# Performance work log

Measured on AMD Instinct MI355X. Metric: run time of the kernel, lower is better.

## Reference

```python
import jax, jax.numpy as jnp
import numpy as np

B, N, F_IN = 256, 256, 128
HID, DEPTH = 48, 4
D_OUT = 97                 # sum(latent_dim [32,32,32,1]) = GraphUNet out_channels
K_SORT = 30
C1, C2, KW2 = 16, 32, 5
POOL_LEN = (K_SORT - 2) // 2 + 1        # 15 after maxpool1d(2,2)
DENSE_DIM = (POOL_LEN - KW2 + 1) * C2   # 352
OUT_DIM = 32


def _gcn(x, A, W, b):
    # GCNConv(improved=True): A_hat = A + 2I; out = D^-1/2 A_hat D^-1/2 (x W) + b
    n = A.shape[-1]
    Ah = A + 2.0 * jnp.eye(n, dtype=A.dtype)
    dinv = jax.lax.rsqrt(jnp.sum(Ah, axis=-1))          # deg >= 2 always
    An = dinv[:, :, None] * Ah * dinv[:, None, :]
    return An @ (x @ W) + b


def _augment(A):
    # GraphUNet.augment_adj: add self loops, two-hop (A@A), remove self loops
    n = A.shape[-1]
    eye = jnp.eye(n, dtype=A.dtype)
    A1 = A + eye
    return (A1 @ A1) * (1.0 - eye)


def _topk_pool(x, A, p):
    # TopKPooling(ratio=0.5, nonlinearity=tanh): score = tanh(x.p/||p||)
    Bb, n, _ = x.shape
    score = jnp.tanh((x @ p) / jnp.sqrt(jnp.sum(p * p)))
    k = (n + 1) // 2
    vals, perm = jax.lax.top_k(score, k)                # [B,k]
    bidx = jnp.arange(Bb)[:, None]
    xp = x[bidx, perm] * vals[..., None]                # gate kept nodes by score
    Ap = A[bidx[..., None], perm[:, :, None], perm[:, None, :]]
    return xp, Ap, perm


def _forward(x, A, dW0, db0, dW, db, pool_p, uW, ub, uWl, ubl, c1W, c1b, c2W, c2b, oW, ob):
    act = jax.nn.relu
    # ---- GraphUNet down path ----
    h = act(_gcn(x, A, dW0, db0))
    xs, As, perms = [h], [A], []
    Acur = A
    for i in range(DEPTH):
        A2 = _augment(Acur)
        h, Acur, perm = _topk_pool(h, A2, pool_p[i])
        h = act(_gcn(h, Acur, dW[i], db[i]))
        if i < DEPTH - 1:
            xs.append(h)
            As.append(Acur)
        perms.append(perm)
    # ---- up path with sum skip connections ----
    for i in range(DEPTH):
        j = DEPTH - 1 - i
        res, Aj, perm = xs[j], As[j], perms[j]
        bidx = jnp.arange(res.shape[0])[:, None]
        up = jnp.zeros_like(res).at[bidx, perm].set(h)
        h = res + up
        if i < DEPTH - 1:
            h = act(_gcn(h, Aj, uW[i], ub[i]))
        else:
            h = _gcn(h, Aj, uWl, ubl)                   # [B,N,D_OUT], no act
    # ---- global_sort_pool: sort nodes by last channel desc, keep top K_SORT ----
    _, order = jax.lax.top_k(h[..., -1], K_SORT)
    sp = h[jnp.arange(B)[:, None], order]               # [B,K_SORT,D_OUT]
    # conv1d(1->C1, kernel=stride=D_OUT) on flattened [B,1,K*D] == per-node linear
    y = jax.nn.relu(jnp.einsum('bkd,cd->bck', sp, c1W) + c1b[None, :, None])  # [B,C1,K]
    y = y.reshape(B, C1, POOL_LEN, 2).max(-1)           # maxpool1d(2,2)
    y = jax.lax.conv_general_dilated(y, c2W, (1,), 'VALID',
                                     dimension_numbers=('NCH', 'OIH', 'NCH'))
    y = jax.nn.relu(y + c2b[None, :, None])             # [B,C2,POOL_LEN-KW2+1]
    return jax.nn.relu(y.reshape(B, -1) @ oW + ob)      # relu(relu(.)) == relu(.)


def setup_inputs():
    key = jax.random.key(0)
    ks = jax.random.split(key, 12)
    x = jax.random.normal(ks[0], (B, N, F_IN), dtype=jnp.float32)
    # symmetric binary adjacency, no self loops, avg degree ~15
    u = jax.random.uniform(ks[1], (B, N, N))
    A = (u < 0.03).astype(jnp.float32)
    A = jnp.maximum(A, A.transpose(0, 2, 1)) * (1.0 - jnp.eye(N, dtype=jnp.float32))
    s = lambda f: np.float32(1.0 / np.sqrt(f))
    return dict(
        x=x, A=A,
        dW0=jax.random.normal(ks[2], (F_IN, HID), dtype=jnp.float32) * s(F_IN),
        db0=jnp.zeros((HID,), jnp.float32),
        dW=jax.random.normal(ks[3], (DEPTH, HID, HID), dtype=jnp.float32) * s(HID),
        db=jnp.zeros((DEPTH, HID), jnp.float32),
        pool_p=jax.random.normal(ks[4], (DEPTH, HID), dtype=jnp.float32) * s(HID),
        uW=jax.random.normal(ks[5], (DEPTH - 1, HID, HID), dtype=jnp.float32) * s(HID),
        ub=jnp.zeros((DEPTH - 1, HID), jnp.float32),
        uWl=jax.random.normal(ks[6], (HID, D_OUT), dtype=jnp.float32) * s(HID),
        ubl=jnp.zeros((D_OUT,), jnp.float32),
        c1W=jax.random.normal(ks[7], (C1, D_OUT), dtype=jnp.float32) * s(D_OUT),
        c1b=jnp.zeros((C1,), jnp.float32),
        c2W=jax.random.normal(ks[8], (C2, C1, KW2), dtype=jnp.float32) * s(C1 * KW2),
        c2b=jnp.zeros((C2,), jnp.float32),
        oW=jax.random.normal(ks[9], (DENSE_DIM, OUT_DIM), dtype=jnp.float32) * s(DENSE_DIM),
        ob=jnp.zeros((OUT_DIM,), jnp.float32),
    )


def reference(x, A, dW0, db0, dW, db, pool_p, uW, ub, uWl, ubl, c1W, c1b, c2W, c2b, oW, ob):
    return _forward(x, A, dW0, db0, dW, db, pool_p, uW, ub, uWl, ubl, c1W, c1b, c2W, c2b, oW, ob)
```

## Files before the change

kernel.cpp:

```cpp
#include <hip/hip_runtime.h>
#include <math.h>

#define BATCH 256
#define NNODE 256
#define FIN   128
#define HID   48
#define DOUT  97

#define WOFF_DW0 0
#define WOFF_DW  6144
#define WOFF_UW  18432
#define WOFF_UWL 27648
#define WTOT     34816

typedef __attribute__((ext_vector_type(8))) short bf16x8_t;
typedef __attribute__((ext_vector_type(4))) float f32x4_t;

__device__ inline unsigned short f2bf(float x) {
  unsigned u = __float_as_uint(x);
  u += 0x7fff + ((u >> 16) & 1);
  return (unsigned short)(u >> 16);
}
__device__ inline float bf2f(unsigned short h) {
  return __uint_as_float(((unsigned)h) << 16);
// ... 77 lines not shown
  int mt = (blockIdx.x * 256 + threadIdx.x) >> 6;
  int lane = threadIdx.x & 63;
  int r = lane & 15, q = lane >> 4;
  const float* xr = X + ((long)mt * 16 + r) * K;
  bf16x8_t ah[KS2], am[KS2], al[KS2];
  #pragma unroll
  for (int ks = 0; ks < KS2; ks++) {
    int col0 = ks * 32 + q * 8;
    float v[8];
    if (col0 + 8 <= K) {
      float4 a = *(const float4*)(xr + col0);
      float4 b = *(const float4*)(xr + col0 + 4);
      v[0] = a.x; v[1] = a.y; v[2] = a.z; v[3] = a.w;
      v[4] = b.x; v[5] = b.y; v[6] = b.z; v[7] = b.w;
    } else {
      #pragma unroll
      for (int j = 0; j < 8; j++) v[j] = (col0 + j < K) ? xr[col0 + j] : 0.f;
    }
    #pragma unroll
    for (int j = 0; j < 8; j++) {
      unsigned short h = f2bf(v[j]);
      float r1 = v[j] - bf2f(h);
      unsigned short m = f2bf(r1);
      float r2 = r1 - bf2f(m);
      unsigned short l = f2bf(r2);
      ah[ks][j] = (short)h;
      am[ks][j] = (short)m;
      al[ks][j] = (short)l;
    }
  }
  long row0 = (long)mt * 16 + q * 4;
  float4 dv4 = {0.f, 0.f, 0.f, 0.f};
  long ytBase = 0;
  if (Yth) {
    dv4 = *(const float4*)(dinv + row0);
    int bb = (int)(row0 >> nShift);
    int jj = (int)(row0 & ((1 << nShift) - 1));
    ytBase = (long)bb * Fpad;
    ytBase = ytBase << nShift;
    ytBase += jj;
  }
  int nFT = Fpad >> 4;
  for (int ft = 0; ft < nFT; ft++) {
    int fl = ft * 16 + r;
    const unsigned short* wb = Wp + (size_t)fl * KP + q * 8;
    f32x4_t acc = {0.f, 0.f, 0.f, 0.f};
    #pragma unroll
    for (int ks = 0; ks < KS2; ks++) {
      bf16x8_t bh = *(const bf16x8_t*)(wb + ks * 32);
      bf16x8_t bm = *(const bf16x8_t*)(wb + WTOT + ks * 32);
      bf16x8_t bl = *(const bf16x8_t*)(wb + 2 * WTOT + ks * 32);
      acc = __builtin_amdgcn_mfma_f32_16x16x32_bf16(ah[ks], bh, acc, 0, 0, 0);
      acc = __builtin_amdgcn_mfma_f32_16x16x32_bf16(ah[ks], bm, acc, 0, 0, 0);
      acc = __builtin_amdgcn_mfma_f32_16x16x32_bf16(am[ks], bh, acc, 0, 0, 0);
      acc = __builtin_amdgcn_mfma_f32_16x16x32_bf16(am[ks], bm, acc, 0, 0, 0);
      acc = __builtin_amdgcn_mfma_f32_16x16x32_bf16(ah[ks], bl, acc, 0, 0, 0);
      acc = __builtin_amdgcn_mfma_f32_16x16x32_bf16(al[ks], bh, acc, 0, 0, 0);
    }
    int f = fl;
    if (f < F) {
      if (XW) {
        #pragma unroll
        for (int reg = 0; reg < 4; reg++) XW[(row0 + reg) * F + f] = acc[reg];
      }
      if (Yth) {
        float dvv[4] = {dv4.x, dv4.y, dv4.z, dv4.w};
        unsigned long long hpk = 0, lpk = 0;
        #pragma unroll
        for (int reg = 0; reg < 4; reg++) {
          float v = dvv[reg] * acc[reg];
          unsigned short hi = f2bf(v);
          unsigned short lo = f2bf(v - bf2f(hi));
          hpk |= ((unsigned long long)hi) << (16 * reg);
          lpk |= ((unsigned long long)lo) << (16 * reg);
        }
        long o = ytBase + ((long)f << nShift);
        *(unsigned long long*)(Yth + o) = hpk;
        *(unsigned long long*)(Ytl + o) = lpk;
      }
    }
  }
}

__global__ __launch_bounds__(512) void k_big(const float* __restrict__ x,
                                             const unsigned short* __restrict__ Wp0,
                                             const unsigned short* __restrict__ Abf0,
                                             const float* __restrict__ D0,
                                             const float* __restrict__ db0,
                                             float* __restrict__ H0) {
  __shared__ __align__(16) char yt0[24576];
  __shared__ __align__(16) char yt1[24576];
  int b = blockIdx.x, t = threadIdx.x;
  int w = t >> 6, lane = t & 63;
  int r = lane & 15, q = lane >> 4;
  const float* Xb = x + (size_t)b * 256 * 128;
  const float* Db = D0 + (size_t)b * 256;
  #pragma unroll
  for (int half = 0; half < 2; half++) {
    int m = w + half * 8;
    const float* xr = Xb + (size_t)(m * 16 + r) * 128;
    bf16x8_t ah[4], am[4], al[4];
    #pragma unroll
    for (int ks = 0; ks < 4; ks++) {
      int col0 = ks * 32 + q * 8;
      float4 a4 = *(const float4*)(xr + col0);
      float4 b4 = *(const float4*)(xr + col0 + 4);
      float v[8] = {a4.x, a4.y, a4.z, a4.w, b4.x, b4.y, b4.z, b4.w};
      #pragma unroll
      for (int j = 0; j < 8; j++) {
        unsigned short h = f2bf(v[j]); float r1 = v[j] - bf2f(h);
        unsigned short mm = f2bf(r1);  float r2 = r1 - bf2f(mm);
        ah[ks][j] = (short)h; am[ks][j] = (short)mm; al[ks][j] = (short)f2bf(r2);
      }
    }
    int row0 = m * 16 + q * 4;
    float4 dv4 = *(const float4*)(Db + row0);
    float dvv[4] = {dv4.x, dv4.y, dv4.z, dv4.w};
    #pragma unroll
    for (int ft = 0; ft < 3; ft++) {
      int fl = ft * 16 + r;
      const unsigned short* wb = Wp0 + (size_t)fl * 128 + q * 8;
      f32x4_t acc = {0.f, 0.f, 0.f, 0.f};
      #pragma unroll
      for (int ks = 0; ks < 4; ks++) {
        bf16x8_t bh = *(const bf16x8_t*)(wb + ks * 32);
        bf16x8_t bm = *(const bf16x8_t*)(wb + WTOT + ks * 32);
        bf16x8_t bl = *(const bf16x8_t*)(wb + 2 * WTOT + ks * 32);
        acc = __builtin_amdgcn_mfma_f32_16x16x32_bf16(ah[ks], bh, acc, 0, 0, 0);
        acc = __builtin_amdgcn_mfma_f32_16x16x32_bf16(ah[ks], bm, acc, 0, 0, 0);
        acc = __builtin_amdgcn_mfma_f32_16x16x32_bf16(am[ks], bh, acc, 0, 0, 0);
        acc = __builtin_amdgcn_mfma_f32_16x16x32_bf16(am[ks], bm, acc, 0, 0, 0);
        acc = __builtin_amdgcn_mfma_f32_16x16x32_bf16(ah[ks], bl, acc, 0, 0, 0);
        acc = __builtin_amdgcn_mfma_f32_16x16x32_bf16(al[ks], bh, acc, 0, 0, 0);
      }
      #pragma unroll
      for (int reg = 0; reg < 4; reg++) {
        float vv = dvv[reg] * acc[reg];
        unsigned short hi = f2bf(vv);
        unsigned short lo = f2bf(vv - bf2f(hi));
        int byte = (fl * 512 + (row0 + reg) * 2) ^ ((fl & 7) << 4);
        *(unsigned short*)(yt0 + byte) = hi;
        *(unsigned short*)(yt1 + byte) = lo;
      }
    }
  }
  __syncthreads();
  #pragma unroll
  for (int half = 0; half < 2; half++) {
    int it = w + half * 8;
    const unsigned short* ap = Abf0 + ((size_t)b * 256 + it * 16 + r) * 256 + q * 8;
    bf16x8_t af[8];
    #pragma unroll
    for (int ks = 0; ks < 8; ks++) af[ks] = *(const bf16x8_t*)(ap + ks * 32);
    #pragma unroll
    for (int ft = 0; ft < 3; ft++) {
      int fl = ft * 16 + r;
      f32x4_t acc = {0.f, 0.f, 0.f, 0.f};
      #pragma unroll
      for (int ks = 0; ks < 8; ks++) {
        int byte = (fl * 512 + (ks * 32 + q * 8) * 2) ^ ((fl & 7) << 4);
        bf16x8_t bh = *(const bf16x8_t*)(yt0 + byte);
        bf16x8_t bl = *(const bf16x8_t*)(yt1 + byte);
        acc = __builtin_amdgcn_mfma_f32_16x16x32_bf16(af[ks], bh, acc, 0, 0, 0);
        acc = __builtin_amdgcn_mfma_f32_16x16x32_bf16(af[ks], bl, acc, 0, 0, 0);
      }
      float bfv = db0[fl];
      #pragma unroll
      for (int reg = 0; reg < 4; reg++) {
        int rr = it * 16 + q * 4 + reg;
        int sbyte = (fl * 512 + rr * 2) ^ ((fl & 7) << 4);
        float selfv = bf2f(*(const unsigned short*)(yt0 + sbyte))
                    + bf2f(*(const unsigned short*)(yt1 + sbyte));
        float d = Db[rr];
        float v = d * acc[reg] + 2.f * d * selfv + bfv;
        H0[((size_t)b * 256 + rr) * 48 + fl] = fmaxf(v, 0.f);
      }
    }
  }
}

template<int MODE>
__device__ inline void gcn128_phase(const float* __restrict__ Xg,
                                    const unsigned short* __restrict__ Wpl,
                                    const unsigned short* __restrict__ A1,
                                    const float* __restrict__ D1b,
                                    const float* __restrict__ bias,
                                    char* yt0, char* yt1,
                                    float* __restrict__ H1,
                                    float* __restrict__ H0b,
                                    const int* sPerm1, int t) {
  int w = t >> 6, lane = t & 63;
  int r = lane & 15, q = lane >> 4;
  {
    const float* xr = Xg + (size_t)(w * 16 + r) * 48;
    bf16x8_t ah[2], am[2], al[2];
    #pragma unroll
    for (int ks = 0; ks < 2; ks++) {
      int col0 = ks * 32 + q * 8;
      float v[8];
      if (col0 + 8 <= 48) {
        float4 a4 = *(const float4*)(xr + col0);
        float4 b4 = *(const float4*)(xr + col0 + 4);
        v[0]=a4.x; v[1]=a4.y; v[2]=a4.z; v[3]=a4.w;
        v[4]=b4.x; v[5]=b4.y; v[6]=b4.z; v[7]=b4.w;
      } else {
        #pragma unroll
        for (int j = 0; j < 8; j++) v[j] = (col0 + j < 48) ? xr[col0 + j] : 0.f;
      }
      #pragma unroll
      for (int j = 0; j < 8; j++) {
        unsigned short h = f2bf(v[j]); float r1 = v[j] - bf2f(h);
        unsigned short mm = f2bf(r1);  float r2 = r1 - bf2f(mm);
        ah[ks][j] = (short)h; am[ks][j] = (short)mm; al[ks][j] = (short)f2bf(r2);
      }
    }
    int row0 = w * 16 + q * 4;
    float4 dv4 = *(const float4*)(D1b + row0);
    float dvv[4] = {dv4.x, dv4.y, dv4.z, dv4.w};
    #pragma unroll
    for (int ft = 0; ft < 3; ft++) {
      int fl = ft * 16 + r;
      const unsigned short* wb = Wpl + (size_t)fl * 64 + q * 8;
      f32x4_t acc = {0.f, 0.f, 0.f, 0.f};
      #pragma unroll
      for (int ks = 0; ks < 2; ks++) {
        bf16x8_t bh = *(const bf16x8_t*)(wb + ks * 32);
        bf16x8_t bm = *(const bf16x8_t*)(wb + WTOT + ks * 32);
        bf16x8_t bl = *(const bf16x8_t*)(wb + 2 * WTOT + ks * 32);
        acc = __builtin_amdgcn_mfma_f32_16x16x32_bf16(ah[ks], bh, acc, 0, 0, 0);
        acc = __builtin_amdgcn_mfma_f32_16x16x32_bf16(ah[ks], bm, acc, 0, 0, 0);
        acc = __builtin_amdgcn_mfma_f32_16x16x32_bf16(am[ks], bh, acc, 0, 0, 0);
        acc = __builtin_amdgcn_mfma_f32_16x16x32_bf16(am[ks], bm, acc, 0, 0, 0);
        acc = __builtin_amdgcn_mfma_f32_16x16x32_bf16(ah[ks], bl, acc, 0, 0, 0);
        acc = __builtin_amdgcn_mfma_f32_16x16x32_bf16(al[ks], bh, acc, 0, 0, 0);
      }
      #pragma unroll
      for (int reg = 0; reg < 4; reg++) {
        float vv = dvv[reg] * acc[reg];
        unsigned short hi = f2bf(vv);
        unsigned short lo = f2bf(vv - bf2f(hi));
        int byte = (fl * 256 + (row0 + reg) * 2) ^ ((fl & 7) << 4);
        *(unsigned short*)(yt0 + byte) = hi;
        *(unsigned short*)(yt1 + byte) = lo;
      }
    }
  }
  __syncthreads();
  {
    const unsigned short* ap = A1 + (size_t)(w * 16 + r) * 128 + q * 8;
    bf16x8_t af[4];
    #pragma unroll
    for (int ks = 0; ks < 4; ks++) af[ks] = *(const bf16x8_t*)(ap + ks * 32);
    #pragma unroll
    for (int ft = 0; ft < 3; ft++) {
      int fl = ft * 16 + r;
      f32x4_t acc = {0.f, 0.f, 0.f, 0.f};
      #pragma unroll
      for (int ks = 0; ks < 4; ks++) {
        int byte = (fl * 256 + (ks * 32 + q * 8) * 2) ^ ((fl & 7) << 4);
        bf16x8_t bh = *(const bf16x8_t*)(yt0 + byte);
        bf16x8_t bl = *(const bf16x8_t*)(yt1 + byte);
        acc = __builtin_amdgcn_mfma_f32_16x16x32_bf16(af[ks], bh, acc, 0, 0, 0);
        acc = __builtin_amdgcn_mfma_f32_16x16x32_bf16(af[ks], bl, acc, 0, 0, 0);
      }
      float bfv = bias[fl];
      #pragma unroll
      for (int reg = 0; reg < 4; reg++) {
        int rr = w * 16 + q * 4 + reg;
        int sbyte = (fl * 256 + rr * 2) ^ ((fl & 7) << 4);
        float selfv = bf2f(*(const unsigned short*)(yt0 + sbyte))
                    + bf2f(*(const unsigned short*)(yt1 + sbyte));
        float d = D1b[rr];
        float v = d * acc[reg] + 2.f * d * selfv + bfv;
        v = fmaxf(v, 0.f);
        if (MODE == 0) H1[(size_t)rr * 48 + fl] = v;
        else {
          int node = sPerm1[rr];
          H0b[(size_t)node * 48 + fl] += v;
        }
      }
    }
  }
  __syncthreads();
}

__device__ inline void xw_dphase(const float* hin, const float* W, const float* dv,
                                 float* xwd, int n, int t) {
  for (int idx = t; idx < n * 48; idx += 512) {
    int j = idx / 48, f = idx - j * 48;
    const float* hr = hin + j * 48;
    float a = 0.f;
    #pragma unroll
    for (int g = 0; g < 48; g++) a += hr[g] * W[g * 48 + f];
    xwd[idx] = dv[j] * a;
  }
}

__device__ inline void anxw_phase(const float* A, int lda, const float* xwd,
                                  const float* dv, const float* bias,
                                  float* hout, int n, int t) {
  for (int idx = t; idx < n * 48; idx += 512) {
    int i = idx / 48, f = idx - i * 48;
    const float* ar = A + i * lda;
    float acc = 0.f;
    #pragma unroll 4
    for (int j = 0; j < n; j++) acc += ar[j] * xwd[j * 48 + f];
    float di = dv[i];
    float v = di * acc + 2.f * di * xwd[i * 48 + f] + bias[f];
    hout[idx] = fmaxf(v, 0.f);
  }
}

template<int N, int K>
__device__ inline void pool_phaseT(const float* h, const float* p,
                                   float* sS, int* perm, float* hin, int t) {
  constexpr int LPR = 512 / N;
  int row = t / LPR, sub = t % LPR;
  float pn = 0.f;
  #pragma unroll
  for (int g = 0; g < 48; g++) pn += p[g] * p[g];
  const float* hr = h + row * 48;
  float acc = 0.f;
  for (int g = sub; g < 48; g += LPR) acc += hr[g] * p[g];
  acc = grp_sum<LPR>(acc);
  if (sub == 0) sS[row] = tanhf(acc / sqrtf(pn));
  __syncthreads();
  {
    float v = sS[row];
    int r = 0;
    for (int j = sub; j < N; j += LPR) {
      float u = sS[j];
      r += (u > v) || (u == v && j < row);
    }
    r = grp_isum<LPR>(r);
    if (sub == 0 && r < K) perm[r] = row;
  }
  __syncthreads();
  for (int idx = t; idx < K * 48; idx += 512) {
    int r = idx / 48, g = idx - r * 48;
    int pi = perm[r];
    hin[idx] = h[pi * 48 + g] * sS[pi];
  }
  __syncthreads();
}

template<int NN, int KK>
__device__ inline void aug_phaseT(const float* A, int lda, const int* perm,
                                  float* Ao, int ldo, float* dout, int t) {
  for (int idx = t; idx < KK * KK; idx += 512) {
    int r = idx / KK, c = idx - r * KK;
    int pr = perm[r], pc = perm[c];
    const float* ra = A + pr * lda;
    const float* rc = A + pc * lda;
    float acc = 0.f;
    #pragma unroll 4
    for (int j = 0; j < NN; j++) acc += ra[j] * rc[j];
    float v = acc + 2.f * ra[pc];
    Ao[r * ldo + c] = (r == c) ? 0.f : v;
  }
  __syncthreads();
  {
    constexpr int LPR = 512 / KK;
    int row = t / LPR, sub = t % LPR;
    float s = 0.f;
    for (int j = sub; j < KK; j += LPR) s += Ao[row * ldo + j];
    s = grp_sum<LPR>(s);
    if (sub == 0) dout[row] = 1.0f / sqrtf(s + 2.0f);
  }
  __syncthreads();
}

__device__ inline void scat_phase(const int* perm, const float* src, float* dst,
                                  int k, int t) {
  for (int idx = t; idx < k * 48; idx += 512) {
    int r = idx / 48, g = idx - r * 48;
    dst[perm[r] * 48 + g] += src[idx];
  }
  __syncthreads();
}

__global__ __launch_bounds__(512) void k_mid(const unsigned short* __restrict__ Abf0,
                                             unsigned short* __restrict__ Abf1g,
                                             float* __restrict__ H0,
                                             float* __restrict__ H1g,
                                             float* __restrict__ D1g,
                                             const unsigned short* __restrict__ Wp,
                                             const float* __restrict__ dW,
                                             const float* __restrict__ dbv,
                                             const float* __restrict__ pp,
                                             const float* __restrict__ uW,
                                             const float* __restrict__ ub) {
  int b = blockIdx.x, t = threadIdx.x;
  __shared__ __align__(16) char arena[63488];
  __shared__ int sPerm1[128];
  float* H1 = H1g + (size_t)b * 128 * 48;
  float* H0b = H0 + (size_t)b * 256 * 48;
  unsigned short* A1 = Abf1g + (size_t)b * 128 * 128;
  float* D1b = D1g + (size_t)b * 128;

  {
    float* sc = (float*)arena;
    const float* p = pp;
    float pn = 0.f;
    #pragma unroll
    for (int g = 0; g < 48; g++) pn += p[g] * p[g];
    int row = t >> 1, sub = t & 1;
    const float* hr = H0b + (size_t)row * 48;
    float a = 0.f;
    for (int g = sub; g < 48; g += 2) a += hr[g] * p[g];
    a = grp_sum<2>(a);
    if (!sub) sc[row] = tanhf(a / sqrtf(pn));
    __syncthreads();
    float vv = sc[row];
    int rk = 0;
    for (int j = sub; j < 256; j += 2) {
      float u = sc[j];
      rk += (u > vv) || (u == vv && j < row);
    }
    rk = grp_isum<2>(rk);
    if (!sub && rk < 128) sPerm1[rk] = row;
    __syncthreads();
    for (int idx = t; idx < 128 * 48; idx += 512) {
      int rr = idx / 48, g = idx - rr * 48;
      int pi = sPerm1[rr];
      H1[idx] = H0b[(size_t)pi * 48 + g] * sc[pi];
    }
  }
  __syncthreads();

  {
    int w = t >> 6, lane = t & 63;
    int r = lane & 15, q = lane >> 4;
    int rowA = sPerm1[w * 16 + r];
    const unsigned short* Ab = Abf0 + (size_t)b * 256 * 256;
    const unsigned short* pa = Ab + (size_t)rowA * 256 + q * 8;
    bf16x8_t af[8];
    #pragma unroll
    for (int ks = 0; ks < 8; ks++) {
      bf16x8_t a = *(const bf16x8_t*)(pa + ks * 32);
      int da = rowA - ks * 32 - q * 8;
      #pragma unroll
      for (int e = 0; e < 8; e++) if (da == e) a[e] = (short)0x3F80;
      af[ks] = a;
    }
    float dsum[4] = {0.f, 0.f, 0.f, 0.f};
    for (int ft = 0; ft < 8; ft++) {
      int rowB = sPerm1[ft * 16 + r];
      const unsigned short* pb = Ab + (size_t)rowB * 256 + q * 8;
      f32x4_t acc = {0.f, 0.f, 0.f, 0.f};
      #pragma unroll
      for (int ks = 0; ks < 8; ks++) {
        bf16x8_t bv = *(const bf16x8_t*)(pb + ks * 32);
        int db_ = rowB - ks * 32 - q * 8;
        #pragma unroll
        for (int e = 0; e < 8; e++) if (db_ == e) bv[e] = (short)0x3F80;
        acc = __builtin_amdgcn_mfma_f32_16x16x32_bf16(af[ks], bv, acc, 0, 0, 0);
      }
      int c = ft * 16 + r;
      #pragma unroll
      for (int reg = 0; reg < 4; reg++) {
        int rr = w * 16 + q * 4 + reg;
        float v = (rr == c) ? 0.f : acc[reg];
        A1[(size_t)rr * 128 + c] = f2bf(v);
        float s = v;
        s += __shfl_xor(s, 1); s += __shfl_xor(s, 2);
        s += __shfl_xor(s, 4); s += __shfl_xor(s, 8);
        dsum[reg] += s;
      }
    }
    if (r == 0) {
      #pragma unroll
      for (int reg = 0; reg < 4; reg++)
        D1b[w * 16 + q * 4 + reg] = 1.0f / sqrtf(dsum[reg] + 2.0f);
    }
  }
  __syncthreads();

  gcn128_phase<0>(H1, Wp + WOFF_DW, A1, D1b, dbv,
                  (char*)arena, (char*)arena + 12288, H1, nullptr, sPerm1, t);

  {
    float* sS  = (float*)(arena);
    int*   sP2 = (int*)(arena + 512);
    int*   sP3 = (int*)(arena + 768);
    int*   sP4 = (int*)(arena + 896);
    float* sD2 = (float*)(arena + 960);
    float* sD3 = (float*)(arena + 1216);
    float* sD4 = (float*)(arena + 1344);
    float* sA2 = (float*)(arena + 1536);
    float* sA3 = (float*)(arena + 18176);
    float* sH2 = (float*)(arena + 22400);
    float* sH3 = (float*)(arena + 34688);
    float* sXW = (float*)(arena + 40832);
    float* hin = (float*)(arena + 53120);
    float* sH4 = (float*)(arena + 59264);
    float* sA4 = (float*)(arena + 62336);

    {
      const float* p = pp + 48;
      float pn = 0.f;
      #pragma unroll
      for (int g = 0; g < 48; g++) pn += p[g] * p[g];
      int row = t >> 2, sub = t & 3;
      const float* hr = H1 + (size_t)row * 48;
      float acc = 0.f;
      for (int g = sub; g < 48; g += 4) acc += hr[g] * p[g];
      acc = grp_sum<4>(acc);
      if (sub == 0) sS[row] = tanhf(acc / sqrtf(pn));
      __syncthreads();
      float v = sS[row];
      int rk = 0;
      for (int j = sub; j < 128; j += 4) {
        float u = sS[j];
        rk += (u > v) || (u == v && j < row);
      }
      rk = grp_isum<4>(rk);
      if (sub == 0 && rk < 64) sP2[rk] = row;
      __syncthreads();
    }
    {
      int w = t >> 6, lane = t & 63;
      int r = lane & 15, q = lane >> 4;
      #pragma unroll
      for (int tt = 0; tt < 2; tt++) {
        int tile = w * 2 + tt;
        int it = tile >> 2, ft = tile & 3;
        int rowA = sP2[it * 16 + r];
        int rowB = sP2[ft * 16 + r];
        const unsigned short* pa = A1 + (size_t)rowA * 128 + q * 8;
        const unsigned short* pb = A1 + (size_t)rowB * 128 + q * 8;
        f32x4_t acc = {0.f, 0.f, 0.f, 0.f};
        #pragma unroll
        for (int k0 = 0; k0 < 128; k0 += 32) {
          bf16x8_t a  = *(const bf16x8_t*)(pa + k0);
          bf16x8_t bv = *(const bf16x8_t*)(pb + k0);
          int daA = rowA - k0 - q * 8;
          int daB = rowB - k0 - q * 8;
          #pragma unroll
          for (int e = 0; e < 8; e++) {
            if (daA == e) a[e] = (short)0x3F80;
            if (daB == e) bv[e] = (short)0x3F80;
          }
          acc = __builtin_amdgcn_mfma_f32_16x16x32_bf16(a, bv, acc, 0, 0, 0);
        }
        int c = ft * 16 + r;
        #pragma unroll
        for (int reg = 0; reg < 4; reg++) {
          int rr = it * 16 + q * 4 + reg;
          sA2[rr * 65 + c] = (rr == c) ? 0.f : acc[reg];
        }
      }
    }
    __syncthreads();
    {
      int row = t >> 3, sub = t & 7;
      float s = 0.f;
      for (int j = sub; j < 64; j += 8) s += sA2[row * 65 + j];
      s = grp_sum<8>(s);
      if (sub == 0) sD2[row] = 1.0f / sqrtf(s + 2.0f);
    }
    __syncthreads();
    for (int idx = t; idx < 64 * 48; idx += 512) {
      int j = idx / 48, f = idx - j * 48;
      int pi = sP2[j];
      const float* hr = H1 + (size_t)pi * 48;
      const float* W = dW + 2304;
      float a = 0.f;
      #pragma unroll
      for (int g = 0; g < 48; g++) a += hr[g] * W[g * 48 + f];
      sXW[idx] = sD2[j] * sS[pi] * a;
    }
    __syncthreads();
    anxw_phase(sA2, 65, sXW, sD2, dbv + 48, sH2, 64, t);
    __syncthreads();

    pool_phaseT<64, 32>(sH2, pp + 96, sS, sP3, hin, t);
    aug_phaseT<64, 32>(sA2, 65, sP3, sA3, 33, sD3, t);
    xw_dphase(hin, dW + 2 * 2304, sD3, sXW, 32, t);
    __syncthreads();
    anxw_phase(sA3, 33, sXW, sD3, dbv + 96, sH3, 32, t);
    __syncthreads();

    pool_phaseT<32, 16>(sH3, pp + 144, sS, sP4, hin, t);
    aug_phaseT<32, 16>(sA3, 33, sP4, sA4, 17, sD4, t);
    xw_dphase(hin, dW + 3 * 2304, sD4, sXW, 16, t);
    __syncthreads();
    anxw_phase(sA4, 17, sXW, sD4, dbv + 144, sH4, 16, t);
    __syncthreads();

    scat_phase(sP4, sH4, sH3, 16, t);
    xw_dphase(sH3, uW, sD3, sXW, 32, t);
    __syncthreads();
    anxw_phase(sA3, 33, sXW, sD3, ub, sH3, 32, t);
    __syncthreads();

    scat_phase(sP3, sH3, sH2, 32, t);
    xw_dphase(sH2, uW + 2304, sD2, sXW, 64, t);
    __syncthreads();
    anxw_phase(sA2, 65, sXW, sD2, ub + 48, sH2, 64, t);
    __syncthreads();

    for (int idx = t; idx < 64 * 48; idx += 512) {
      int r2 = idx / 48, g = idx - r2 * 48;
      H1[(size_t)sP2[r2] * 48 + g] += sH2[idx];
    }
  }
  __syncthreads();

  gcn128_phase<1>(H1, Wp + WOFF_UW + 2 * 3072, A1, D1b, ub + 96,
                  (char*)arena, (char*)arena + 12288, nullptr, H0b, sPerm1, t);
}

__global__ __launch_bounds__(512) void k_htail(const unsigned short* __restrict__ Abf,
                                               const float* __restrict__ dinv,
                                               const unsigned short* __restrict__ Yth,
                                               const unsigned short* __restrict__ Ytl,
                                               const float* __restrict__ ubl,
                                               float* __restrict__ sp) {
  int b = blockIdx.x, t = threadIdx.x;
  __shared__ float sy[256];
  __shared__ float sc[256];
  __shared__ int sord[32];
  const unsigned short* yh = Yth + ((size_t)b * 112 + 96) * 256;
  const unsigned short* yl = Ytl + ((size_t)b * 112 + 96) * 256;
  if (t < 256) sy[t] = bf2f(yh[t]) + bf2f(yl[t]);
  __syncthreads();
  {
    int i = t >> 1, sub = t & 1;
    const unsigned short* ar = Abf + ((size_t)b * 256 + i) * 256 + sub * 128;
    const float* syp = sy + sub * 128;
    float s = 0.f;
    for (int j = 0; j < 128; j += 2) {
      unsigned u = *(const unsigned*)(ar + j);
      s += bf2f((unsigned short)(u & 0xffffu)) * syp[j]
         + bf2f((unsigned short)(u >> 16)) * syp[j + 1];
    }
    s += __shfl_xor(s, 1);
    if (sub == 0) {
      float d = dinv[(size_t)b * 256 + i];
      sc[i] = d * s + 2.f * d * sy[i];
    }
  }
  __syncthreads();
  {
    int i = t >> 1, sub = t & 1;
    float v = sc[i];
    int r = 0;
    int j0 = sub * 128;
    for (int j = j0; j < j0 + 128; j++) {
      float u = sc[j];
      r += (u > v) || (u == v && j < i);
    }
    r += __shfl_xor(r, 1);
    if (sub == 0 && r < 30) sord[r] = i;
  }
  __syncthreads();
  int wave = t >> 6, lane = t & 63;
  int it = wave & 1, fh = wave >> 1;
  int r = lane & 15, q = lane >> 4;
  int ari = it * 16 + r;
  int arow = sord[ari < 30 ? ari : 0];
  const unsigned short* ap = Abf + ((size_t)b * 256 + arow) * 256 + q * 8;
  bf16x8_t af[8];
  #pragma unroll
  for (int ks = 0; ks < 8; ks++) af[ks] = *(const bf16x8_t*)(ap + ks * 32);
  int ftBeg = fh * 2, ftEnd = fh * 2 + 2;
  if (ftEnd > 7) ftEnd = 7;
  for (int ft = ftBeg; ft < ftEnd; ft++) {
    int fl = ft * 16 + r;
    const unsigned short* yrowh = Yth + ((size_t)b * 112 + fl) * 256;
    const unsigned short* yrowl = Ytl + ((size_t)b * 112 + fl) * 256;
    f32x4_t acc = {0.f, 0.f, 0.f, 0.f};
    #pragma unroll
    for (int ks = 0; ks < 8; ks++) {
      bf16x8_t bh = *(const bf16x8_t*)(yrowh + q * 8 + ks * 32);
      bf16x8_t bl = *(const bf16x8_t*)(yrowl + q * 8 + ks * 32);
      acc = __builtin_amdgcn_mfma_f32_16x16x32_bf16(af[ks], bh, acc, 0, 0, 0);
      acc = __builtin_amdgcn_mfma_f32_16x16x32_bf16(af[ks], bl, acc, 0, 0, 0);
    }
    if (fl < DOUT) {
      float bf = ubl[fl];
      #pragma unroll
      for (int reg = 0; reg < 4; reg++) {
        int rowidx = it * 16 + q * 4 + reg;
        if (rowidx < 30) {
          int node = sord[rowidx];
          float d = dinv[(size_t)b * 256 + node];
          float yv = bf2f(yrowh[node]) + bf2f(yrowl[node]);
          sp[((size_t)b * 30 + rowidx) * DOUT + fl] = d * acc[reg] + 2.f * d * yv + bf;
        }
      }
    }
  }
}

__global__ __launch_bounds__(256) void k_head2(const float* __restrict__ spg,
                                               const float* __restrict__ c1W,
                                               const float* __restrict__ c1b,
                                               const float* __restrict__ c2W,
                                               const float* __restrict__ c2b,
                                               const float* __restrict__ oW,
                                               const float* __restrict__ ob,
                                               float* __restrict__ out) {
  int b = blockIdx.x, t = threadIdx.x;
  __shared__ float sp[30 * 97];
  __shared__ float y1[16 * 30];
  __shared__ float yp[16 * 15];
  __shared__ float yc[32 * 11];
  __shared__ float red[256];
  const float* spb = spg + (size_t)b * 30 * 97;
  for (int idx = t; idx < 30 * 97; idx += 256) sp[idx] = spb[idx];
  __syncthreads();
  for (int idx = t; idx < 16 * 30; idx += 256) {
    int c = idx / 30, kk = idx - c * 30;
    float a = c1b[c];
    for (int d = 0; d < 97; d++) a += sp[kk * 97 + d] * c1W[c * 97 + d];
    y1[c * 30 + kk] = fmaxf(a, 0.f);
  }
  __syncthreads();
  for (int idx = t; idx < 16 * 15; idx += 256) {
    int c = idx / 15, t2 = idx - c * 15;
    yp[idx] = fmaxf(y1[c * 30 + 2 * t2], y1[c * 30 + 2 * t2 + 1]);
  }
  __syncthreads();
  for (int idx = t; idx < 32 * 11; idx += 256) {
    int o = idx / 11, t3 = idx - o * 11;
    float a = c2b[o];
    for (int i2 = 0; i2 < 16; i2++)
      for (int w = 0; w < 5; w++)
        a += yp[i2 * 15 + t3 + w] * c2W[(o * 16 + i2) * 5 + w];
    yc[o * 11 + t3] = fmaxf(a, 0.f);
  }
  __syncthreads();
  {
    int o = t & 31, g = t >> 5;
    float a = 0.f;
    for (int qq = g * 44; qq < g * 44 + 44; qq++) a += yc[qq] * oW[qq * 32 + o];
    red[t] = a;
  }
  __syncthreads();
  if (t < 32) {
    float a = ob[t];
    #pragma unroll
    for (int g = 0; g < 8; g++) a += red[t + 32 * g];
    out[(size_t)b * 32 + t] = fmaxf(a, 0.f);
  }
}

extern "C" void kernel_launch(void* const* d_in, const int* in_sizes, int n_in,
                              void* d_out, int out_size, void* d_ws, size_t ws_size,
                              hipStream_t stream) {
  const float* x   = (const float*)d_in[0];
  const float* A0  = (const float*)d_in[1];
  const float* dW0 = (const float*)d_in[2];
  const float* db0 = (const float*)d_in[3];
  const float* dW  = (const float*)d_in[4];
  const float* dbv = (const float*)d_in[5];
  const float* pp  = (const float*)d_in[6];
  const float* uW  = (const float*)d_in[7];
  const float* ub  = (const float*)d_in[8];
  const float* uWl = (const float*)d_in[9];
  const float* ubl = (const float*)d_in[10];
  const float* c1W = (const float*)d_in[11];
  const float* c1b = (const float*)d_in[12];
  const float* c2W = (const float*)d_in[13];
  const float* c2b = (const float*)d_in[14];
  const float* oW  = (const float*)d_in[15];
  const float* ob  = (const float*)d_in[16];
  float* out = (float*)d_out;

  float* base = (float*)d_ws;
  size_t off = 0;
  auto alloc = [&](size_t nel) { nel = (nel + 3) & ~(size_t)3; float* p = base + off; off += nel; return p; };
  float* H0 = alloc((size_t)BATCH * 256 * HID);
  float* H1 = alloc((size_t)BATCH * 128 * HID);
  float* D0 = alloc((size_t)BATCH * 256);
  float* D1 = alloc((size_t)BATCH * 128);
  float* SP = alloc((size_t)BATCH * 30 * 97);
  unsigned short* Abf0 = (unsigned short*)alloc((size_t)BATCH * 256 * 256 / 2);
  unsigned short* Abf1 = (unsigned short*)alloc((size_t)BATCH * 128 * 128 / 2);
  unsigned short* Yth  = (unsigned short*)alloc((size_t)BATCH * 112 * 256 / 2);
  unsigned short* Ytl  = (unsigned short*)alloc((size_t)BATCH * 112 * 256 / 2);
  unsigned short* Wp   = (unsigned short*)alloc((size_t)3 * WTOT / 2 + 4);

  k_prepA<<<BATCH * 256 / 4, 256, 0, stream>>>(A0, Abf0, D0, BATCH * 256);
  k_splitW3<<<(WTOT + 255) / 256, 256, 0, stream>>>(dW0, dW, uW, uWl, Wp);

  k_big<<<BATCH, 512, 0, stream>>>(x, Wp + WOFF_DW0, Abf0, D0, db0, H0);

  k_mid<<<BATCH, 512, 0, stream>>>(Abf0, Abf1, H0, H1, D1, Wp, dW, dbv, pp, uW, ub);

  k_xws<2><<<BATCH * 256 / 64, 256, 0, stream>>>(H0, Wp + WOFF_UWL, nullptr,
                                                 D0, Yth, Ytl, HID, DOUT, 112, 8);
  k_htail<<<BATCH, 512, 0, stream>>>(Abf0, D0, Yth, Ytl, ubl, SP);

  k_head2<<<BATCH, 256, 0, stream>>>(SP, c1W, c1b, c2W, c2b, oW, ob, out);
}
```

Measured before the change: 423.6 us.

## Double per-graph block size to 1024 threads and redistribute wave tasks

Launches the per-graph kernels k_big, k_mid and k_htail with 1024 threads instead of 512. Every phase is re-partitioned so each wave handles fewer row/feature tiles, and reductions and rank counts use wider lane groups. The degree computation for the first pooled adjacency moves from shuffle reductions inside the MFMA loop to a separate pass over the stored bf16 matrix. The aim is more parallelism per graph to hide latency, at the cost of tighter register limits per thread, an extra barrier, and some waves idle in phases with few tiles.

```diff
diff --git a/kernel.cpp b/kernel.cpp
--- a/kernel.cpp
+++ b/kernel.cpp
@@ -183,12 +183,12 @@
   }
 }
 
-__global__ __launch_bounds__(512) void k_big(const float* __restrict__ x,
-                                             const unsigned short* __restrict__ Wp0,
-                                             const unsigned short* __restrict__ Abf0,
-                                             const float* __restrict__ D0,
-                                             const float* __restrict__ db0,
-                                             float* __restrict__ H0) {
+__global__ __launch_bounds__(1024) void k_big(const float* __restrict__ x,
+                                              const unsigned short* __restrict__ Wp0,
+                                              const unsigned short* __restrict__ Abf0,
+                                              const float* __restrict__ D0,
+                                              const float* __restrict__ db0,
+                                              float* __restrict__ H0) {
   __shared__ __align__(16) char yt0[24576];
   __shared__ __align__(16) char yt1[24576];
   int b = blockIdx.x, t = threadIdx.x;
@@ -196,9 +196,8 @@
   int r = lane & 15, q = lane >> 4;
   const float* Xb = x + (size_t)b * 256 * 128;
   const float* Db = D0 + (size_t)b * 256;
-  #pragma unroll
-  for (int half = 0; half < 2; half++) {
-    int m = w + half * 8;
+  {
+    int m = w;
     const float* xr = Xb + (size_t)(m * 16 + r) * 128;
     bf16x8_t ah[4], am[4], al[4];
     #pragma unroll
@@ -246,9 +245,8 @@
     }
   }
   __syncthreads();
-  #pragma unroll
-  for (int half = 0; half < 2; half++) {
-    int it = w + half * 8;
+  {
+    int it = w;
     const unsigned short* ap = Abf0 + ((size_t)b * 256 + it * 16 + r) * 256 + q * 8;
     bf16x8_t af[8];
     #pragma unroll
@@ -292,8 +290,9 @@
                                     const int* sPerm1, int t) {
   int w = t >> 6, lane = t & 63;
   int r = lane & 15, q = lane >> 4;
-  {
-    const float* xr = Xg + (size_t)(w * 16 + r) * 48;
+  for (int task = w; task < 24; task += 16) {
+    int m = task / 3, ft = task - m * 3;
+    const float* xr = Xg + (size_t)(m * 16 + r) * 48;
     bf16x8_t ah[2], am[2], al[2];
     #pragma unroll
     for (int ks = 0; ks < 2; ks++) {
@@ -315,70 +314,65 @@
         ah[ks][j] = (short)h; am[ks][j] = (short)mm; al[ks][j] = (short)f2bf(r2);
       }
     }
-    int row0 = w * 16 + q * 4;
+    int row0 = m * 16 + q * 4;
     float4 dv4 = *(const float4*)(D1b + row0);
     float dvv[4] = {dv4.x, dv4.y, dv4.z, dv4.w};
-    #pragma unroll
-    for (int ft = 0; ft < 3; ft++) {
-      int fl = ft * 16 + r;
-      const unsigned short* wb = Wpl + (size_t)fl * 64 + q * 8;
-      f32x4_t acc = {0.f, 0.f, 0.f, 0.f};
-      #pragma unroll
-      for (int ks = 0; ks < 2; ks++) {
-        bf16x8_t bh = *(const bf16x8_t*)(wb + ks * 32);
-        bf16x8_t bm = *(const bf16x8_t*)(wb + WTOT + ks * 32);
-        bf16x8_t bl = *(const bf16x8_t*)(wb + 2 * WTOT + ks * 32);
-        acc = __builtin_amdgcn_mfma_f32_16x16x32_bf16(ah[ks], bh, acc, 0, 0, 0);
-        acc = __builtin_amdgcn_mfma_f32_16x16x32_bf16(ah[ks], bm, acc, 0, 0, 0);
-        acc = __builtin_amdgcn_mfma_f32_16x16x32_bf16(am[ks], bh, acc, 0, 0, 0);
-        acc = __builtin_amdgcn_mfma_f32_16x16x32_bf16(am[ks], bm, acc, 0, 0, 0);
-        acc = __builtin_amdgcn_mfma_f32_16x16x32_bf16(ah[ks], bl, acc, 0, 0, 0);
-        acc = __builtin_amdgcn_mfma_f32_16x16x32_bf16(al[ks], bh, acc, 0, 0, 0);
-      }
-      #pragma unroll
-      for (int reg = 0; reg < 4; reg++) {
-        float vv = dvv[reg] * acc[reg];
-        unsigned short hi = f2bf(vv);
-        unsigned short lo = f2bf(vv - bf2f(hi));
-        int byte = (fl * 256 + (row0 + reg) * 2) ^ ((fl & 7) << 4);
-        *(unsigned short*)(yt0 + byte) = hi;
-        *(unsigned short*)(yt1 + byte) = lo;
-      }
-    }
-  }
-  __syncthreads();
-  {
-    const unsigned short* ap = A1 + (size_t)(w * 16 + r) * 128 + q * 8;
+    int fl = ft * 16 + r;
+    const unsigned short* wb = Wpl + (size_t)fl * 64 + q * 8;
+    f32x4_t acc = {0.f, 0.f, 0.f, 0.f};
+    #pragma unroll
+    for (int ks = 0; ks < 2; ks++) {
+      bf16x8_t bh = *(const bf16x8_t*)(wb + ks * 32);
+      bf16x8_t bm = *(const bf16x8_t*)(wb + WTOT + ks * 32);
+      bf16x8_t bl = *(const bf16x8_t*)(wb + 2 * WTOT + ks * 32);
+      acc = __builtin_amdgcn_mfma_f32_16x16x32_bf16(ah[ks], bh, acc, 0, 0, 0);
+      acc = __builtin_amdgcn_mfma_f32_16x16x32_bf16(ah[ks], bm, acc, 0, 0, 0);
+      acc = __builtin_amdgcn_mfma_f32_16x16x32_bf16(am[ks], bh, acc, 0, 0, 0);
+      acc = __builtin_amdgcn_mfma_f32_16x16x32_bf16(am[ks], bm, acc, 0, 0, 0);
+      acc = __builtin_amdgcn_mfma_f32_16x16x32_bf16(ah[ks], bl, acc, 0, 0, 0);
+      acc = __builtin_amdgcn_mfma_f32_16x16x32_bf16(al[ks], bh, acc, 0, 0, 0);
+    }
+    #pragma unroll
+    for (int reg = 0; reg < 4; reg++) {
+      float vv = dvv[reg] * acc[reg];
+      unsigned short hi = f2bf(vv);
+      unsigned short lo = f2bf(vv - bf2f(hi));
+      int byte = (fl * 256 + (row0 + reg) * 2) ^ ((fl & 7) << 4);
+      *(unsigned short*)(yt0 + byte) = hi;
+      *(unsigned short*)(yt1 + byte) = lo;
+    }
+  }
+  __syncthreads();
+  for (int task = w; task < 24; task += 16) {
+    int it = task / 3, ft = task - it * 3;
+    const unsigned short* ap = A1 + (size_t)(it * 16 + r) * 128 + q * 8;
     bf16x8_t af[4];
     #pragma unroll
     for (int ks = 0; ks < 4; ks++) af[ks] = *(const bf16x8_t*)(ap + ks * 32);
-    #pragma unroll
-    for (int ft = 0; ft < 3; ft++) {
-      int fl = ft * 16 + r;
-      f32x4_t acc = {0.f, 0.f, 0.f, 0.f};
-      #pragma unroll
-      for (int ks = 0; ks < 4; ks++) {
-        int byte = (fl * 256 + (ks * 32 + q * 8) * 2) ^ ((fl & 7) << 4);
-        bf16x8_t bh = *(const bf16x8_t*)(yt0 + byte);
-        bf16x8_t bl = *(const bf16x8_t*)(yt1 + byte);
-        acc = __builtin_amdgcn_mfma_f32_16x16x32_bf16(af[ks], bh, acc, 0, 0, 0);
-        acc = __builtin_amdgcn_mfma_f32_16x16x32_bf16(af[ks], bl, acc, 0, 0, 0);
-      }
-      float bfv = bias[fl];
-      #pragma unroll
-      for (int reg = 0; reg < 4; reg++) {
-        int rr = w * 16 + q * 4 + reg;
-        int sbyte = (fl * 256 + rr * 2) ^ ((fl & 7) << 4);
-        float selfv = bf2f(*(const unsigned short*)(yt0 + sbyte))
-                    + bf2f(*(const unsigned short*)(yt1 + sbyte));
-        float d = D1b[rr];
-        float v = d * acc[reg] + 2.f * d * selfv + bfv;
-        v = fmaxf(v, 0.f);
-        if (MODE == 0) H1[(size_t)rr * 48 + fl] = v;
-        else {
-          int node = sPerm1[rr];
-          H0b[(size_t)node * 48 + fl] += v;
-        }
+    int fl = ft * 16 + r;
+    f32x4_t acc = {0.f, 0.f, 0.f, 0.f};
+    #pragma unroll
+    for (int ks = 0; ks < 4; ks++) {
+      int byte = (fl * 256 + (ks * 32 + q * 8) * 2) ^ ((fl & 7) << 4);
+      bf16x8_t bh = *(const bf16x8_t*)(yt0 + byte);
+      bf16x8_t bl = *(const bf16x8_t*)(yt1 + byte);
+      acc = __builtin_amdgcn_mfma_f32_16x16x32_bf16(af[ks], bh, acc, 0, 0, 0);
+      acc = __builtin_amdgcn_mfma_f32_16x16x32_bf16(af[ks], bl, acc, 0, 0, 0);
+    }
+    float bfv = bias[fl];
+    #pragma unroll
+    for (int reg = 0; reg < 4; reg++) {
+      int rr = it * 16 + q * 4 + reg;
+      int sbyte = (fl * 256 + rr * 2) ^ ((fl & 7) << 4);
+      float selfv = bf2f(*(const unsigned short*)(yt0 + sbyte))
+                  + bf2f(*(const unsigned short*)(yt1 + sbyte));
+      float d = D1b[rr];
+      float v = d * acc[reg] + 2.f * d * selfv + bfv;
+      v = fmaxf(v, 0.f);
+      if (MODE == 0) H1[(size_t)rr * 48 + fl] = v;
+      else {
+        int node = sPerm1[rr];
+        H0b[(size_t)node * 48 + fl] += v;
       }
     }
   }
@@ -387,7 +381,7 @@
 
 __device__ inline void xw_dphase(const float* hin, const float* W, const float* dv,
                                  float* xwd, int n, int t) {
-  for (int idx = t; idx < n * 48; idx += 512) {
+  for (int idx = t; idx < n * 48; idx += 1024) {
     int j = idx / 48, f = idx - j * 48;
     const float* hr = hin + j * 48;
     float a = 0.f;
@@ -400,7 +394,7 @@
 __device__ inline void anxw_phase(const float* A, int lda, const float* xwd,
                                   const float* dv, const float* bias,
                                   float* hout, int n, int t) {
-  for (int idx = t; idx < n * 48; idx += 512) {
+  for (int idx = t; idx < n * 48; idx += 1024) {
     int i = idx / 48, f = idx - i * 48;
     const float* ar = A + i * lda;
     float acc = 0.f;
@@ -415,7 +409,7 @@
 template<int N, int K>
 __device__ inline void pool_phaseT(const float* h, const float* p,
                                    float* sS, int* perm, float* hin, int t) {
-  constexpr int LPR = 512 / N;
+  constexpr int LPR = 1024 / N;
   int row = t / LPR, sub = t % LPR;
   float pn = 0.f;
   #pragma unroll
@@ -437,7 +431,7 @@
     if (sub == 0 && r < K) perm[r] = row;
   }
   __syncthreads();
-  for (int idx = t; idx < K * 48; idx += 512) {
+  for (int idx = t; idx < K * 48; idx += 1024) {
     int r = idx / 48, g = idx - r * 48;
     int pi = perm[r];
     hin[idx] = h[pi * 48 + g] * sS[pi];
@@ -448,7 +442,7 @@
 template<int NN, int KK>
 __device__ inline void aug_phaseT(const float* A, int lda, const int* perm,
                                   float* Ao, int ldo, float* dout, int t) {
-  for (int idx = t; idx < KK * KK; idx += 512) {
+  for (int idx = t; idx < KK * KK; idx += 1024) {
     int r = idx / KK, c = idx - r * KK;
     int pr = perm[r], pc = perm[c];
     const float* ra = A + pr * lda;
@@ -461,11 +455,11 @@
   }
   __syncthreads();
   {
-    constexpr int LPR = 512 / KK;
+    constexpr int LPR = 1024 / KK;
     int row = t / LPR, sub = t % LPR;
     float s = 0.f;
     for (int j = sub; j < KK; j += LPR) s += Ao[row * ldo + j];
-    s = grp_sum<LPR>(s);
+    s = grp_sum<(LPR > 64 ? 64 : LPR)>(s);
     if (sub == 0) dout[row] = 1.0f / sqrtf(s + 2.0f);
   }
   __syncthreads();
@@ -473,24 +467,24 @@
 
 __device__ inline void scat_phase(const int* perm, const float* src, float* dst,
                                   int k, int t) {
-  for (int idx = t; idx < k * 48; idx += 512) {
+  for (int idx = t; idx < k * 48; idx += 1024) {
     int r = idx / 48, g = idx - r * 48;
     dst[perm[r] * 48 + g] += src[idx];
   }
   __syncthreads();
 }
 
-__global__ __launch_bounds__(512) void k_mid(const unsigned short* __restrict__ Abf0,
-                                             unsigned short* __restrict__ Abf1g,
-                                             float* __restrict__ H0,
-                                             float* __restrict__ H1g,
-                                             float* __restrict__ D1g,
-                                             const unsigned short* __restrict__ Wp,
-                                             const float* __restrict__ dW,
-                                             const float* __restrict__ dbv,
-                                             const float* __restrict__ pp,
-                                             const float* __restrict__ uW,
-                                             const float* __restrict__ ub) {
+__global__ __launch_bounds__(1024) void k_mid(const unsigned short* __restrict__ Abf0,
+                                              unsigned short* __restrict__ Abf1g,
+                                              float* __restrict__ H0,
+                                              float* __restrict__ H1g,
+                                              float* __restrict__ D1g,
+                                              const unsigned short* __restrict__ Wp,
+                                              const float* __restrict__ dW,
+                                              const float* __restrict__ dbv,
+                                              const float* __restrict__ pp,
+                                              const float* __restrict__ uW,
+                                              const float* __restrict__ ub) {
   int b = blockIdx.x, t = threadIdx.x;
   __shared__ __align__(16) char arena[63488];
   __shared__ int sPerm1[128];
@@ -505,23 +499,23 @@
     float pn = 0.f;
     #pragma unroll
     for (int g = 0; g < 48; g++) pn += p[g] * p[g];
-    int row = t >> 1, sub = t & 1;
+    int row = t >> 2, sub = t & 3;
     const float* hr = H0b + (size_t)row * 48;
     float a = 0.f;
-    for (int g = sub; g < 48; g += 2) a += hr[g] * p[g];
-    a = grp_sum<2>(a);
+    for (int g = sub; g < 48; g += 4) a += hr[g] * p[g];
+    a = grp_sum<4>(a);
     if (!sub) sc[row] = tanhf(a / sqrtf(pn));
     __syncthreads();
     float vv = sc[row];
     int rk = 0;
-    for (int j = sub; j < 256; j += 2) {
+    for (int j = sub; j < 256; j += 4) {
       float u = sc[j];
       rk += (u > vv) || (u == vv && j < row);
     }
-    rk = grp_isum<2>(rk);
+    rk = grp_isum<4>(rk);
     if (!sub && rk < 128) sPerm1[rk] = row;
     __syncthreads();
-    for (int idx = t; idx < 128 * 48; idx += 512) {
+    for (int idx = t; idx < 128 * 48; idx += 1024) {
       int rr = idx / 48, g = idx - rr * 48;
       int pi = sPerm1[rr];
       H1[idx] = H0b[(size_t)pi * 48 + g] * sc[pi];
@@ -532,7 +526,8 @@
   {
     int w = t >> 6, lane = t & 63;
     int r = lane & 15, q = lane >> 4;
-    int rowA = sPerm1[w * 16 + r];
+    int it = w >> 1, fh = w & 1;
+    int rowA = sPerm1[it * 16 + r];
     const unsigned short* Ab = Abf0 + (size_t)b * 256 * 256;
     const unsigned short* pa = Ab + (size_t)rowA * 256 + q * 8;
     bf16x8_t af[8];
@@ -544,8 +539,7 @@
       for (int e = 0; e < 8; e++) if (da == e) a[e] = (short)0x3F80;
       af[ks] = a;
     }
-    float dsum[4] = {0.f, 0.f, 0.f, 0.f};
-    for (int ft = 0; ft < 8; ft++) {
+    for (int ft = fh * 4; ft < fh * 4 + 4; ft++) {
       int rowB = sPerm1[ft * 16 + r];
       const unsigned short* pb = Ab + (size_t)rowB * 256 + q * 8;
       f32x4_t acc = {0.f, 0.f, 0.f, 0.f};
@@ -560,20 +554,23 @@
       int c = ft * 16 + r;
       #pragma unroll
       for (int reg = 0; reg < 4; reg++) {
-        int rr = w * 16 + q * 4 + reg;
+        int rr = it * 16 + q * 4 + reg;
         float v = (rr == c) ? 0.f : acc[reg];
         A1[(size_t)rr * 128 + c] = f2bf(v);
-        float s = v;
-        s += __shfl_xor(s, 1); s += __shfl_xor(s, 2);
-        s += __shfl_xor(s, 4); s += __shfl_xor(s, 8);
-        dsum[reg] += s;
-      }
-    }
-    if (r == 0) {
-      #pragma unroll
-      for (int reg = 0; reg < 4; reg++)
-        D1b[w * 16 + q * 4 + reg] = 1.0f / sqrtf(dsum[reg] + 2.0f);
-    }
+      }
+    }
+  }
+  __syncthreads();
+  {
+    int row = t >> 3, sub = t & 7;
+    const unsigned* ar = (const unsigned*)(A1 + (size_t)row * 128);
+    float s = 0.f;
+    for (int jj = sub; jj < 64; jj += 8) {
+      unsigned u = ar[jj];
+      s += bf2f((unsigned short)(u & 0xffffu)) + bf2f((unsigned short)(u >> 16));
+    }
+    s = grp_sum<8>(s);
+    if (sub == 0) D1b[row] = 1.0f / sqrtf(s + 2.0f);
   }
   __syncthreads();
 
@@ -602,66 +599,62 @@
       float pn = 0.f;
       #pragma unroll
       for (int g = 0; g < 48; g++) pn += p[g] * p[g];
-      int row = t >> 2, sub = t & 3;
+      int row = t >> 3, sub = t & 7;
       const float* hr = H1 + (size_t)row * 48;
       float acc = 0.f;
-      for (int g = sub; g < 48; g += 4) acc += hr[g] * p[g];
-      acc = grp_sum<4>(acc);
+      for (int g = sub; g < 48; g += 8) acc += hr[g] * p[g];
+      acc = grp_sum<8>(acc);
       if (sub == 0) sS[row] = tanhf(acc / sqrtf(pn));
       __syncthreads();
       float v = sS[row];
       int rk = 0;
-      for (int j = sub; j < 128; j += 4) {
+      for (int j = sub; j < 128; j += 8) {
         float u = sS[j];
         rk += (u > v) || (u == v && j < row);
       }
-      rk = grp_isum<4>(rk);
+      rk = grp_isum<8>(rk);
       if (sub == 0 && rk < 64) sP2[rk] = row;
       __syncthreads();
     }
     {
       int w = t >> 6, lane = t & 63;
       int r = lane & 15, q = lane >> 4;
-      #pragma unroll
-      for (int tt = 0; tt < 2; tt++) {
-        int tile = w * 2 + tt;
-        int it = tile >> 2, ft = tile & 3;
-        int rowA = sP2[it * 16 + r];
-        int rowB = sP2[ft * 16 + r];
-        const unsigned short* pa = A1 + (size_t)rowA * 128 + q * 8;
-        const unsigned short* pb = A1 + (size_t)rowB * 128 + q * 8;
-        f32x4_t acc = {0.f, 0.f, 0.f, 0.f};
+      int it = w >> 2, ft = w & 3;
+      int rowA = sP2[it * 16 + r];
+      int rowB = sP2[ft * 16 + r];
+      const unsigned short* pa = A1 + (size_t)rowA * 128 + q * 8;
+      const unsigned short* pb = A1 + (size_t)rowB * 128 + q * 8;
+      f32x4_t acc = {0.f, 0.f, 0.f, 0.f};
+      #pragma unroll
+      for (int k0 = 0; k0 < 128; k0 += 32) {
+        bf16x8_t a  = *(const bf16x8_t*)(pa + k0);
+        bf16x8_t bv = *(const bf16x8_t*)(pb + k0);
+        int daA = rowA - k0 - q * 8;
+        int daB = rowB - k0 - q * 8;
         #pragma unroll
-        for (int k0 = 0; k0 < 128; k0 += 32) {
-          bf16x8_t a  = *(const bf16x8_t*)(pa + k0);
-          bf16x8_t bv = *(const bf16x8_t*)(pb + k0);
-          int daA = rowA - k0 - q * 8;
-          int daB = rowB - k0 - q * 8;
-          #pragma unroll
-          for (int e = 0; e < 8; e++) {
-            if (daA == e) a[e] = (short)0x3F80;
-            if (daB == e) bv[e] = (short)0x3F80;
-          }
-          acc = __builtin_amdgcn_mfma_f32_16x16x32_bf16(a, bv, acc, 0, 0, 0);
+        for (int e = 0; e < 8; e++) {
+          if (daA == e) a[e] = (short)0x3F80;
+          if (daB == e) bv[e] = (short)0x3F80;
         }
-        int c = ft * 16 + r;
-        #pragma unroll
-        for (int reg = 0; reg < 4; reg++) {
-          int rr = it * 16 + q * 4 + reg;
-          sA2[rr * 65 + c] = (rr == c) ? 0.f : acc[reg];
-        }
+        acc = __builtin_amdgcn_mfma_f32_16x16x32_bf16(a, bv, acc, 0, 0, 0);
+      }
+      int c = ft * 16 + r;
+      #pragma unroll
+      for (int reg = 0; reg < 4; reg++) {
+        int rr = it * 16 + q * 4 + reg;
+        sA2[rr * 65 + c] = (rr == c) ? 0.f : acc[reg];
       }
     }
     __syncthreads();
     {
-      int row = t >> 3, sub = t & 7;
+      int row = t >> 4, sub = t & 15;
       float s = 0.f;
-      for (int j = sub; j < 64; j += 8) s += sA2[row * 65 + j];
-      s = grp_sum<8>(s);
+      for (int j = sub; j < 64; j += 16) s += sA2[row * 65 + j];
+      s = grp_sum<16>(s);
       if (sub == 0) sD2[row] = 1.0f / sqrtf(s + 2.0f);
     }
     __syncthreads();
-    for (int idx = t; idx < 64 * 48; idx += 512) {
+    for (int idx = t; idx < 64 * 48; idx += 1024) {
       int j = idx / 48, f = idx - j * 48;
       int pi = sP2[j];
       const float* hr = H1 + (size_t)pi * 48;
@@ -701,7 +694,7 @@
     anxw_phase(sA2, 65, sXW, sD2, ub + 48, sH2, 64, t);
     __syncthreads();
 
-    for (int idx = t; idx < 64 * 48; idx += 512) {
+    for (int idx = t; idx < 64 * 48; idx += 1024) {
       int r2 = idx / 48, g = idx - r2 * 48;
       H1[(size_t)sP2[r2] * 48 + g] += sH2[idx];
     }
@@ -712,12 +705,12 @@
                   (char*)arena, (char*)arena + 12288, nullptr, H0b, sPerm1, t);
 }
 
-__global__ __launch_bounds__(512) void k_htail(const unsigned short* __restrict__ Abf,
-                                               const float* __restrict__ dinv,
-                                               const unsigned short* __restrict__ Yth,
-                                               const unsigned short* __restrict__ Ytl,
-                                               const float* __restrict__ ubl,
-                                               float* __restrict__ sp) {
+__global__ __launch_bounds__(1024) void k_htail(const unsigned short* __restrict__ Abf,
+                                                const float* __restrict__ dinv,
+                                                const unsigned short* __restrict__ Yth,
+                                                const unsigned short* __restrict__ Ytl,
+                                                const float* __restrict__ ubl,
+                                                float* __restrict__ sp) {
   int b = blockIdx.x, t = threadIdx.x;
   __shared__ float sy[256];
   __shared__ float sc[256];
@@ -727,16 +720,16 @@
   if (t < 256) sy[t] = bf2f(yh[t]) + bf2f(yl[t]);
   __syncthreads();
   {
-    int i = t >> 1, sub = t & 1;
-    const unsigned short* ar = Abf + ((size_t)b * 256 + i) * 256 + sub * 128;
-    const float* syp = sy + sub * 128;
+    int i = t >> 2, sub = t & 3;
+    const unsigned short* ar = Abf + ((size_t)b * 256 + i) * 256 + sub * 64;
+    const float* syp = sy + sub * 64;
     float s = 0.f;
-    for (int j = 0; j < 128; j += 2) {
+    for (int j = 0; j < 64; j += 2) {
       unsigned u = *(const unsigned*)(ar + j);
       s += bf2f((unsigned short)(u & 0xffffu)) * syp[j]
          + bf2f((unsigned short)(u >> 16)) * syp[j + 1];
     }
-    s += __shfl_xor(s, 1);
+    s = grp_sum<4>(s);
     if (sub == 0) {
       float d = dinv[(size_t)b * 256 + i];
       sc[i] = d * s + 2.f * d * sy[i];
@@ -744,30 +737,28 @@
   }
   __syncthreads();
   {
-    int i = t >> 1, sub = t & 1;
+    int i = t >> 2, sub = t & 3;
     float v = sc[i];
-    int r = 0;
-    int j0 = sub * 128;
-    for (int j = j0; j < j0 + 128; j++) {
+    int rk = 0;
+    int j0 = sub * 64;
+    for (int j = j0; j < j0 + 64; j++) {
       float u = sc[j];
-      r += (u > v) || (u == v && j < i);
-    }
-    r += __shfl_xor(r, 1);
-    if (sub == 0 && r < 30) sord[r] = i;
-  }
-  __syncthreads();
-  int wave = t >> 6, lane = t & 63;
-  int it = wave & 1, fh = wave >> 1;
-  int r = lane & 15, q = lane >> 4;
-  int ari = it * 16 + r;
-  int arow = sord[ari < 30 ? ari : 0];
-  const unsigned short* ap = Abf + ((size_t)b * 256 + arow) * 256 + q * 8;
-  bf16x8_t af[8];
-  #pragma unroll
-  for (int ks = 0; ks < 8; ks++) af[ks] = *(const bf16x8_t*)(ap + ks * 32);
-  int ftBeg = fh * 2, ftEnd = fh * 2 + 2;
-  if (ftEnd > 7) ftEnd = 7;
-  for (int ft = ftBeg; ft < ftEnd; ft++) {
+      rk += (u > v) || (u == v && j < i);
+    }
+    rk = grp_isum<4>(rk);
+    if (sub == 0 && rk < 30) sord[rk] = i;
+  }
+  __syncthreads();
+  int w = t >> 6, lane = t & 63;
+  if (w < 14) {
+    int it = w / 7, ft = w % 7;
+    int r = lane & 15, q = lane >> 4;
+    int ari = it * 16 + r;
+    int arow = sord[ari < 30 ? ari : 0];
+    const unsigned short* ap = Abf + ((size_t)b * 256 + arow) * 256 + q * 8;
+    bf16x8_t af[8];
+    #pragma unroll
+    for (int ks = 0; ks < 8; ks++) af[ks] = *(const bf16x8_t*)(ap + ks * 32);
     int fl = ft * 16 + r;
     const unsigned short* yrowh = Yth + ((size_t)b * 112 + fl) * 256;
     const unsigned short* yrowl = Ytl + ((size_t)b * 112 + fl) * 256;
@@ -887,13 +878,13 @@
   k_prepA<<<BATCH * 256 / 4, 256, 0, stream>>>(A0, Abf0, D0, BATCH * 256);
   k_splitW3<<<(WTOT + 255) / 256, 256, 0, stream>>>(dW0, dW, uW, uWl, Wp);
 
-  k_big<<<BATCH, 512, 0, stream>>>(x, Wp + WOFF_DW0, Abf0, D0, db0, H0);
-
-  k_mid<<<BATCH, 512, 0, stream>>>(Abf0, Abf1, H0, H1, D1, Wp, dW, dbv, pp, uW, ub);
+  k_big<<<BATCH, 1024, 0, stream>>>(x, Wp + WOFF_DW0, Abf0, D0, db0, H0);
+
+  k_mid<<<BATCH, 1024, 0, stream>>>(Abf0, Abf1, H0, H1, D1, Wp, dW, dbv, pp, uW, ub);
 
   k_xws<2><<<BATCH * 256 / 64, 256, 0, stream>>>(H0, Wp + WOFF_UWL, nullptr,
                                                  D0, Yth, Ytl, HID, DOUT, 112, 8);
-  k_htail<<<BATCH, 512, 0, stream>>>(Abf0, D0, Yth, Ytl, ubl, SP);
+  k_htail<<<BATCH, 1024, 0, stream>>>(Abf0, D0, Yth, Ytl, ubl, SP);
 
   k_head2<<<BATCH, 256, 0, stream>>>(SP, c1W, c1b, c2W, c2b, oW, ob, out);
 }
```

After: 356.0 us, median of 2. -15.9%, faster.
